# Kernel tuning notes

Measured on AMD Instinct MI355X. Metric: run time of the kernel, lower is better.

The kernel has to match this reference:

```python
import jax, jax.numpy as jnp
import numpy as np

VOCAB, HIDDEN, BATCH, EMB, SEQ = 512, 512, 64, 256, 1024


def _lstm_cell(x, h, c, Wih, Whh, bih, bhh):
    # PyTorch LSTMCell gate order: i, f, g, o
    gates = x @ Wih.T + bih + h @ Whh.T + bhh  # [B, 4H]
    i, f, g, o = jnp.split(gates, 4, axis=-1)
    i = jax.nn.sigmoid(i)
    f = jax.nn.sigmoid(f)
    g = jnp.tanh(g)
    o = jax.nn.sigmoid(o)
    c_new = f * c + i * g
    h_new = o * jnp.tanh(c_new)
    return h_new, c_new


def setup_inputs() -> dict:
    key = jax.random.key(0)
    ks = jax.random.split(key, 12)
    s_e = 1.0 / np.sqrt(HIDDEN)
    inp = {
        "x": jax.random.randint(ks[0], (SEQ, BATCH), 0, VOCAB, dtype=jnp.int64)
        if jax.config.jax_enable_x64 else jax.random.randint(ks[0], (SEQ, BATCH), 0, VOCAB, dtype=jnp.int32),
        "h0": jnp.zeros((BATCH, HIDDEN), jnp.float32),
        "c0": jnp.zeros((BATCH, HIDDEN), jnp.float32),
        "emb": jax.random.normal(ks[1], (VOCAB, EMB), jnp.float32),
        "Wih1": jax.random.uniform(ks[2], (4 * HIDDEN, EMB), jnp.float32, -s_e, s_e),
        "Whh1": jax.random.uniform(ks[3], (4 * HIDDEN, HIDDEN), jnp.float32, -s_e, s_e),
        "bih1": jax.random.uniform(ks[4], (4 * HIDDEN,), jnp.float32, -s_e, s_e),
        "bhh1": jax.random.uniform(ks[5], (4 * HIDDEN,), jnp.float32, -s_e, s_e),
        "Wih2": jax.random.uniform(ks[6], (4 * HIDDEN, HIDDEN), jnp.float32, -s_e, s_e),
        "Whh2": jax.random.uniform(ks[7], (4 * HIDDEN, HIDDEN), jnp.float32, -s_e, s_e),
        "bih2": jax.random.uniform(ks[8], (4 * HIDDEN,), jnp.float32, -s_e, s_e),
        "bhh2": jax.random.uniform(ks[9], (4 * HIDDEN,), jnp.float32, -s_e, s_e),
        "Wfc": jax.random.uniform(ks[10], (VOCAB, HIDDEN), jnp.float32, -s_e, s_e),
        "bfc": jax.random.uniform(ks[11], (VOCAB,), jnp.float32, -s_e, s_e),
    }
    return inp


def reference(x, h0, c0, emb, Wih1, Whh1, bih1, bhh1, Wih2, Whh2, bih2, bhh2, Wfc, bfc):
    # Embedding lookup for the whole sequence: [S, B, E]
    x_emb = emb[x]

    def step(carry, xt):
        h1, c1, h2, c2 = carry
        h1, c1 = _lstm_cell(xt, h1, c1, Wih1, Whh1, bih1, bhh1)
        h2, c2 = _lstm_cell(h1, h2, c2, Wih2, Whh2, bih2, bhh2)
        return (h1, c1, h2, c2), h2

    # Both layers start from the same (h0, c0), matching the original hc1, hc2 = (hc, hc)
    _, h2_seq = jax.lax.scan(step, (h0, c0, h0, c0), x_emb)  # [S, B, H]
    # Dropout is identity in eval mode; output projection over all timesteps at once.
    out = jnp.einsum('sbh,vh->sbv', h2_seq, Wfc) + bfc  # [S, B, V]
    return out
```

## Files before the change

### kernel.cpp

```cpp
#include <hip/hip_runtime.h>

#define SEQn   1024
#define BATCHn 64
#define EMBn   256
#define HIDn   512
#define VOCn   512

#define NGRP 4
#define NL1g 16
#define NL2g 16
#define NFCg 16
#define GBLK (NL1g + NL2g + NFCg)
#define NBLK (NGRP * GBLK)
#define NPHASE (SEQn + 2)
#define HS 8192
#define NSLOT 4
#define THR_IGN (-1)

using f16   = _Float16;
using half8 = __attribute__((ext_vector_type(8))) _Float16;
using f32x4 = __attribute__((ext_vector_type(4))) float;
using i32x4 = __attribute__((ext_vector_type(4))) int;

#define WS_FLG 0
#define WS_H1  4096
#define WS_H2  (WS_H1 + NGRP * NSLOT * 2 * HS * 2)
#define WS_P1  (WS_H2 + NGRP * NSLOT * 2 * HS * 2)


__device__ __forceinline__ float sigm_(float v) { return 1.0f / (1.0f + __expf(-v)); }
__device__ __forceinline__ float tanh_(float v) { return 1.0f - 2.0f / (__expf(2.0f * v) + 1.0f); }

__device__ __forceinline__ void st_b128_sc1(f16* p, f32x4 v) {
  asm volatile("global_store_dwordx4 %0, %1, off sc1" :: "v"(p), "v"(v) : "memory");
}

__device__ __forceinline__ void ld2_sc1(const f16* base, half8 (&a)[2]) {
  f32x4 t0, t1;
  asm volatile(
    "global_load_dwordx4 %0, %2, off sc1\n\t"
    "global_load_dwordx4 %1, %2, off offset:1024 sc1\n\t"
    "s_waitcnt vmcnt(0)"
    : "=&v"(t0), "=&v"(t1) : "v"(base) : "memory");
  a[0] = __builtin_bit_cast(half8, t0);
  a[1] = __builtin_bit_cast(half8, t1);
}
__device__ __forceinline__ void ld4_sc1(const f16* base, half8 (&a)[4]) {
  f32x4 t0, t1, t2, t3;
  asm volatile(
    "global_load_dwordx4 %0, %4, off sc1\n\t"
    "global_load_dwordx4 %1, %4, off offset:1024 sc1\n\t"
    "global_load_dwordx4 %2, %4, off offset:2048 sc1\n\t"
    "global_load_dwordx4 %3, %4, off offset:3072 sc1\n\t"
    "s_waitcnt vmcnt(0)"
    : "=&v"(t0), "=&v"(t1), "=&v"(t2), "=&v"(t3) : "v"(base) : "memory");
  a[0] = __builtin_bit_cast(half8, t0);
  a[1] = __builtin_bit_cast(half8, t1);
  a[2] = __builtin_bit_cast(half8, t2);
  a[3] = __builtin_bit_cast(half8, t3);
}

__global__ void k_init(const float* __restrict__ h0, char* __restrict__ ws) {
  int i = blockIdx.x * 256 + threadIdx.x;
  f16* h1b = (f16*)(ws + WS_H1);
  f16* h2b = (f16*)(ws + WS_H2);
  int g = i >> 13;
  int off = i & (HS - 1);
  int ks = off >> 9, rem = off & 511;
  int qq = rem >> 7, cc = (rem >> 3) & 15, e = rem & 7;
  int row = g * 16 + cc, col = ks * 32 + qq * 8 + e;
  f16 v = (f16)h0[row * HIDn + col];
  int base = g * (NSLOT * 2 * HS);
  h1b[base + off] = v;  h1b[base + HS + off] = v;
  h2b[base + off] = v;  h2b[base + HS + off] = v;
  if (i < 256) ((int*)ws)[i] = 0;
}

__global__ void k_p1(const float* __restrict__ emb, const float* __restrict__ Wih1,
                     const float* __restrict__ bih1, const float* __restrict__ bhh1,
                     char* __restrict__ ws) {
  __shared__ float elds[32 * 256];
  int tid = threadIdx.x;
  int vb = blockIdx.x >> 5, gb = blockIdx.x & 31;
  for (int i = tid; i < 32 * 256; i += 256) elds[i] = emb[vb * 32 * 256 + i];
  __syncthreads();
  int gl = tid & 63, vs = tid >> 6;
  int g = gb * 64 + gl;
  float bias = bih1[g] + bhh1[g];
  float acc[8];
#pragma unroll
  for (int r = 0; r < 8; ++r) acc[r] = bias;
  const float* wrow = Wih1 + g * EMBn;
#pragma unroll 4
  for (int e = 0; e < EMBn; ++e) {
    float w = wrow[e];
#pragma unroll
    for (int r = 0; r < 8; ++r) acc[r] += elds[(vs * 8 + r) * 256 + e] * w;
  }
  f16* P1 = (f16*)(ws + WS_P1);
#pragma unroll
  for (int r = 0; r < 8; ++r) P1[(vb * 32 + vs * 8 + r) * 2048 + g] = (f16)acc[r];
}

__global__ void __launch_bounds__(512, 2)
k_lstm(const int* __restrict__ x, const float* __restrict__ c0,
       const float* __restrict__ Whh1,
       const float* __restrict__ Wih2, const float* __restrict__ Whh2,
       const float* __restrict__ bih2, const float* __restrict__ bhh2,
       const float* __restrict__ Wfc, const float* __restrict__ bfc,
       float* __restrict__ out, char* __restrict__ ws)
{
  __shared__ float part[8][16][132];
  __shared__ alignas(16) f16 hstage[16][32];

  const int bid = blockIdx.x, tid = threadIdx.x;
  const int lane = tid & 63, wv = tid >> 6;
  const int cc = lane & 15, qq = lane >> 4;
  const int group = bid / GBLK, role = bid % GBLK;

  f16* h1g = (f16*)(ws + WS_H1) + group * (NSLOT * 2 * HS);
  f16* h2g = (f16*)(ws + WS_H2) + group * (NSLOT * 2 * HS);
  const f16* P1 = (const f16*)(ws + WS_P1);
  const int cls = (role < NL1g) ? 0 : (role < NL1g + NL2g) ? 1 : 2;
  int* flagp = (int*)ws + (group << 6) + (cls << 4) + (role & 15);

  half8 bfr[32];
  float cst = 0.f;
  float biasr[4] = {0.f, 0.f, 0.f, 0.f};
  float bfcr = 0.f;
  float pgf[4] = {0.f, 0.f, 0.f, 0.f};
  int j0 = 0;
  const int erow = tid >> 5, eu = tid & 31;

  if (cls == 0) {
    j0 = role * 32;
#pragma unroll
    for (int nt = 0; nt < 8; ++nt) {
      const float* wr = Whh1 + ((nt >> 1) * 512 + j0 + (nt & 1) * 16 + cc) * HIDn;
#pragma unroll
      for (int kk = 0; kk < 2; ++kk) {
        const float* s = wr + (wv * 2 + kk) * 32 + qq * 8;
        half8 hv;
#pragma unroll
        for (int j = 0; j < 8; ++j) hv[j] = (f16)s[j];
        bfr[nt * 2 + kk] = hv;
      }
    }
    cst = c0[(group * 16 + erow) * HIDn + j0 + eu];
    {
      const f16* pr = P1 + (size_t)x[group * 16 + erow] * 2048 + j0 + eu;
#pragma unroll
      for (int g = 0; g < 4; ++g) pgf[g] = (float)pr[g * 512];
    }
  } else if (cls == 1) {
    j0 = (role - NL1g) * 32;
    const int kh = wv >> 2, kq = wv & 3;
    const float* W = kh ? Whh2 : Wih2;
#pragma unroll
    for (int nt = 0; nt < 8; ++nt) {
      const float* wr = W + ((nt >> 1) * 512 + j0 + (nt & 1) * 16 + cc) * HIDn;
#pragma unroll
      for (int kk = 0; kk < 4; ++kk) {
        const float* s = wr + (kq * 4 + kk) * 32 + qq * 8;
        half8 hv;
#pragma unroll
        for (int j = 0; j < 8; ++j) hv[j] = (f16)s[j];
        bfr[nt * 4 + kk] = hv;
      }
    }
#pragma unroll
    for (int g = 0; g < 4; ++g)
      biasr[g] = bih2[g * 512 + j0 + eu] + bhh2[g * 512 + j0 + eu];
    cst = c0[(group * 16 + erow) * HIDn + j0 + eu];
  } else {
    j0 = (role - NL1g - NL2g) * 32;
#pragma unroll
    for (int nt = 0; nt < 2; ++nt) {
      const float* wr = Wfc + (j0 + nt * 16 + cc) * HIDn;
#pragma unroll
      for (int kk = 0; kk < 2; ++kk) {
        const float* s = wr + (wv * 2 + kk) * 32 + qq * 8;
        half8 hv;
#pragma unroll
        for (int j = 0; j < 8; ++j) hv[j] = (f16)s[j];
        bfr[nt * 2 + kk] = hv;
      }
    }
    bfcr = bfc[j0 + eu];
  }
  const int ks0 = j0 >> 5;
  __syncthreads();

  for (int p = 1; p <= NPHASE; ++p) {
    if (cls == 0) {
      if (p <= SEQn) {
        const f16* hp = h1g + ((p - 1) & 3) * (2 * HS);
        half8 a[2];
        ld2_sc1(hp + wv * 1024 + lane * 8, a);
        f32x4 acc[8];
#pragma unroll
        for (int nt = 0; nt < 8; ++nt)
#pragma unroll
          for (int r = 0; r < 4; ++r) acc[nt][r] = 0.f;
#pragma unroll
        for (int kk = 0; kk < 2; ++kk)
#pragma unroll
          for (int nt = 0; nt < 8; ++nt)
            acc[nt] = __builtin_amdgcn_mfma_f32_16x16x32_f16(a[kk], bfr[nt * 2 + kk], acc[nt], 0, 0, 0);
#pragma unroll
        for (int nt = 0; nt < 8; ++nt)
#pragma unroll
          for (int r = 0; r < 4; ++r)
            part[wv][qq * 4 + r][nt * 16 + cc] = acc[nt][r];
        __syncthreads();
        {
          float gs[4];
#pragma unroll
          for (int g = 0; g < 4; ++g) {
            float s = pgf[g];
#pragma unroll
            for (int kw = 0; kw < 8; ++kw) s += part[kw][erow][g * 32 + eu];
            gs[g] = s;
          }
          float cn = sigm_(gs[1]) * cst + sigm_(gs[0]) * tanh_(gs[2]);
          cst = cn;
          hstage[erow][eu] = (f16)(sigm_(gs[3]) * tanh_(cn));
        }
        __syncthreads();
        if (tid < 64) {
          f32x4 w = *(const f32x4*)&hstage[tid & 15][(tid >> 4) * 8];
          f16* ho = h1g + (p & 3) * (2 * HS) + ks0 * 512 + tid * 8;
          st_b128_sc1(ho, w);
          st_b128_sc1(ho + HS, w);
        }
      }
    } else if (cls == 1) {
      if (p >= 2 && p <= SEQn + 1) {
        const int kh = wv >> 2, kq = wv & 3;
        const f16* src = kh ? h2g + ((p - 2) & 3) * (2 * HS)
                            : h1g + ((p - 1) & 3) * (2 * HS) + HS;
        half8 a[4];
        ld4_sc1(src + kq * 2048 + lane * 8, a);
        f32x4 acc[8];
#pragma unroll
        for (int nt = 0; nt < 8; ++nt)
#pragma unroll
          for (int r = 0; r < 4; ++r) acc[nt][r] = 0.f;
#pragma unroll
        for (int kk = 0; kk < 4; ++kk)
#pragma unroll
          for (int nt = 0; nt < 8; ++nt)
            acc[nt] = __builtin_amdgcn_mfma_f32_16x16x32_f16(a[kk], bfr[nt * 4 + kk], acc[nt], 0, 0, 0);
#pragma unroll
        for (int nt = 0; nt < 8; ++nt)
#pragma unroll
          for (int r = 0; r < 4; ++r)
            part[wv][qq * 4 + r][nt * 16 + cc] = acc[nt][r];
        __syncthreads();
        {
          float gs[4];
#pragma unroll
          for (int g = 0; g < 4; ++g) {
            float s = biasr[g];
#pragma unroll
            for (int kw = 0; kw < 8; ++kw) s += part[kw][erow][g * 32 + eu];
            gs[g] = s;
          }
          float cn = sigm_(gs[1]) * cst + sigm_(gs[0]) * tanh_(gs[2]);
          cst = cn;
          hstage[erow][eu] = (f16)(sigm_(gs[3]) * tanh_(cn));
        }
        __syncthreads();
        if (tid < 64) {
          f32x4 w = *(const f32x4*)&hstage[tid & 15][(tid >> 4) * 8];
          f16* ho = h2g + ((p - 1) & 3) * (2 * HS) + ks0 * 512 + tid * 8;
          st_b128_sc1(ho, w);
          st_b128_sc1(ho + HS, w);
        }
      }
    } else {
      if (p >= 3) {
        const f16* hp = h2g + ((p - 2) & 3) * (2 * HS) + HS;
        half8 a[2];
        ld2_sc1(hp + wv * 1024 + lane * 8, a);
        f32x4 acc[2];
#pragma unroll
        for (int nt = 0; nt < 2; ++nt)
#pragma unroll
          for (int r = 0; r < 4; ++r) acc[nt][r] = 0.f;
#pragma unroll
        for (int kk = 0; kk < 2; ++kk)
#pragma unroll
          for (int nt = 0; nt < 2; ++nt)
            acc[nt] = __builtin_amdgcn_mfma_f32_16x16x32_f16(a[kk], bfr[nt * 2 + kk], acc[nt], 0, 0, 0);
#pragma unroll
        for (int nt = 0; nt < 2; ++nt)
#pragma unroll
          for (int r = 0; r < 4; ++r)
            part[wv][qq * 4 + r][nt * 16 + cc] = acc[nt][r];
        __syncthreads();
        {
          float s = bfcr;
#pragma unroll
          for (int kw = 0; kw < 8; ++kw) s += part[kw][erow][eu];
          float* op = out + (size_t)(p - 3) * (BATCHn * VOCn)
                    + (group * 16 + erow) * VOCn + j0 + eu;
          __builtin_nontemporal_store(s, op);
        }
      }
    }

    if (tid == 0) {
      if (cls != 2) asm volatile("s_waitcnt vmcnt(0)" ::: "memory");
      asm volatile("global_store_dword %0, %1, off sc1" :: "v"(flagp), "v"(p) : "memory");
    }
    if (cls == 0 && p < SEQn) {
      const f16* pr = P1 + (size_t)x[p * 64 + group * 16 + erow] * 2048 + j0 + eu;
#pragma unroll
      for (int g = 0; g < 4; ++g) pgf[g] = (float)pr[g * 512];
    }
    if (wv == 0) {
      int line = lane >> 2;
      int lc = (line < 3) ? line : 0;
      const int* fp = (const int*)ws + (group << 6) + (lc << 4) + ((lane & 3) << 2);
      int thr;
      if (cls == 0)      thr = (line == 0) ? p : (line == 1 ? p - 2 : THR_IGN);
      else if (cls == 1) thr = (line == 0) ? p : (line == 1 ? p : (line == 2 ? p - 2 : THR_IGN));
      else               thr = (line == 1) ? p : THR_IGN;
      if (line >= 3) thr = THR_IGN;
      for (;;) {
        i32x4 f;
        asm volatile("global_load_dwordx4 %0, %1, off sc1\n\ts_waitcnt vmcnt(0)"
                     : "=v"(f) : "v"(fp) : "memory");
        int ok = (f[0] >= thr) & (f[1] >= thr) & (f[2] >= thr) & (f[3] >= thr);
        if (__all(ok)) break;
        __builtin_amdgcn_s_sleep(1);
      }
    }
    __syncthreads();
  }
}

extern "C" void kernel_launch(void* const* d_in, const int* in_sizes, int n_in,
                              void* d_out, int out_size, void* d_ws, size_t ws_size,
                              hipStream_t stream) {
  (void)in_sizes; (void)n_in; (void)out_size; (void)ws_size;
  const int*   x    = (const int*)  d_in[0];
  const float* h0   = (const float*)d_in[1];
  const float* c0   = (const float*)d_in[2];
  const float* emb  = (const float*)d_in[3];
  const float* Wih1 = (const float*)d_in[4];
  const float* Whh1 = (const float*)d_in[5];
  const float* bih1 = (const float*)d_in[6];
  const float* bhh1 = (const float*)d_in[7];
  const float* Wih2 = (const float*)d_in[8];
  const float* Whh2 = (const float*)d_in[9];
  const float* bih2 = (const float*)d_in[10];
  const float* bhh2 = (const float*)d_in[11];
  const float* Wfc  = (const float*)d_in[12];
  const float* bfc  = (const float*)d_in[13];
  char* ws = (char*)d_ws;

  hipLaunchKernelGGL(k_init, dim3(128), dim3(256), 0, stream, h0, ws);
  hipLaunchKernelGGL(k_p1,   dim3(512), dim3(256), 0, stream, emb, Wih1, bih1, bhh1, ws);
  hipLaunchKernelGGL(k_lstm, dim3(NBLK), dim3(512), 0, stream,
                     x, c0, Whh1, Wih2, Whh2, bih2, bhh2, Wfc, bfc,
                     (float*)d_out, ws);
}
```

Measured before the change: 4.951 ms.

## Deepen hidden-state ring, drop duplicate stores, and make every wave poll flags independently

The hidden-state ring grows from 4 double-copied slots to 8 single-copy slots, and the anti-overwrite wait on consumers is relaxed from p-2 to p-6. Each block now reuses its own freshly computed slice from shared memory instead of waiting on its own flag. All waves poll the flags themselves instead of wave 0 followed by a block barrier. The flag store and h store rotate across waves, and the flag store no longer waits on vmcnt. The goal is to cut per-step barrier and handshake latency on the recurrent critical path. The risk is memory-ordering problems, since the flag may become visible before the h data from other lanes or waves.

After: 6.525 ms. +31.8%, slower.

```diff
diff --git a/kernel.cpp b/kernel.cpp
--- a/kernel.cpp
+++ b/kernel.cpp
@@ -14,7 +14,7 @@
 #define NBLK (NGRP * GBLK)
 #define NPHASE (SEQn + 2)
 #define HS 8192
-#define NSLOT 4
+#define NSLOT 8
 #define THR_IGN (-1)
 
 using f16   = _Float16;
@@ -24,8 +24,8 @@
 
 #define WS_FLG 0
 #define WS_H1  4096
-#define WS_H2  (WS_H1 + NGRP * NSLOT * 2 * HS * 2)
-#define WS_P1  (WS_H2 + NGRP * NSLOT * 2 * HS * 2)
+#define WS_H2  (WS_H1 + NGRP * NSLOT * HS * 2)
+#define WS_P1  (WS_H2 + NGRP * NSLOT * HS * 2)
 
 
 __device__ __forceinline__ float sigm_(float v) { return 1.0f / (1.0f + __expf(-v)); }
@@ -70,9 +70,9 @@
   int qq = rem >> 7, cc = (rem >> 3) & 15, e = rem & 7;
   int row = g * 16 + cc, col = ks * 32 + qq * 8 + e;
   f16 v = (f16)h0[row * HIDn + col];
-  int base = g * (NSLOT * 2 * HS);
-  h1b[base + off] = v;  h1b[base + HS + off] = v;
-  h2b[base + off] = v;  h2b[base + HS + off] = v;
+  int base = g * (NSLOT * HS);
+  h1b[base + off] = v;
+  h2b[base + off] = v;
   if (i < 256) ((int*)ws)[i] = 0;
 }
 
@@ -118,11 +118,12 @@
   const int cc = lane & 15, qq = lane >> 4;
   const int group = bid / GBLK, role = bid % GBLK;
 
-  f16* h1g = (f16*)(ws + WS_H1) + group * (NSLOT * 2 * HS);
-  f16* h2g = (f16*)(ws + WS_H2) + group * (NSLOT * 2 * HS);
+  f16* h1g = (f16*)(ws + WS_H1) + group * (NSLOT * HS);
+  f16* h2g = (f16*)(ws + WS_H2) + group * (NSLOT * HS);
   const f16* P1 = (const f16*)(ws + WS_P1);
   const int cls = (role < NL1g) ? 0 : (role < NL1g + NL2g) ? 1 : 2;
-  int* flagp = (int*)ws + (group << 6) + (cls << 4) + (role & 15);
+  const int owni = role & 15;
+  int* flagp = (int*)ws + (group << 6) + (cls << 4) + owni;
 
   half8 bfr[32];
   float cst = 0.f;
@@ -192,11 +193,18 @@
   __syncthreads();
 
   for (int p = 1; p <= NPHASE; ++p) {
-    if (cls == 0) {
-      if (p <= SEQn) {
-        const f16* hp = h1g + ((p - 1) & 3) * (2 * HS);
+    const int act = (cls == 0) ? (p <= SEQn)
+                  : (cls == 1) ? (p >= 2 && p <= SEQn + 1)
+                               : (p >= 3);
+    if (act) {
+      if (cls == 0) {
+        const f16* hp = h1g + ((p - 1) & 7) * HS;
         half8 a[2];
         ld2_sc1(hp + wv * 1024 + lane * 8, a);
+        if (p >= 2 && wv == (ks0 >> 1)) {
+          half8 sub = *(const half8*)&hstage[cc][qq * 8];
+          if ((ks0 & 1) == 0) a[0] = sub; else a[1] = sub;
+        }
         f32x4 acc[8];
 #pragma unroll
         for (int nt = 0; nt < 8; ++nt)
@@ -212,35 +220,20 @@
 #pragma unroll
           for (int r = 0; r < 4; ++r)
             part[wv][qq * 4 + r][nt * 16 + cc] = acc[nt][r];
-        __syncthreads();
-        {
-          float gs[4];
-#pragma unroll
-          for (int g = 0; g < 4; ++g) {
-            float s = pgf[g];
-#pragma unroll
-            for (int kw = 0; kw < 8; ++kw) s += part[kw][erow][g * 32 + eu];
-            gs[g] = s;
-          }
-          float cn = sigm_(gs[1]) * cst + sigm_(gs[0]) * tanh_(gs[2]);
-          cst = cn;
-          hstage[erow][eu] = (f16)(sigm_(gs[3]) * tanh_(cn));
-        }
-        __syncthreads();
-        if (tid < 64) {
-          f32x4 w = *(const f32x4*)&hstage[tid & 15][(tid >> 4) * 8];
-          f16* ho = h1g + (p & 3) * (2 * HS) + ks0 * 512 + tid * 8;
-          st_b128_sc1(ho, w);
-          st_b128_sc1(ho + HS, w);
-        }
-      }
-    } else if (cls == 1) {
-      if (p >= 2 && p <= SEQn + 1) {
+      } else if (cls == 1) {
         const int kh = wv >> 2, kq = wv & 3;
-        const f16* src = kh ? h2g + ((p - 2) & 3) * (2 * HS)
-                            : h1g + ((p - 1) & 3) * (2 * HS) + HS;
+        const f16* src = kh ? h2g + ((p - 2) & 7) * HS
+                            : h1g + ((p - 1) & 7) * HS;
         half8 a[4];
         ld4_sc1(src + kq * 2048 + lane * 8, a);
+        if (p >= 3 && kh == 1 && kq == (ks0 >> 2)) {
+          half8 sub = *(const half8*)&hstage[cc][qq * 8];
+          int k3 = ks0 & 3;
+          if (k3 == 0) a[0] = sub;
+          else if (k3 == 1) a[1] = sub;
+          else if (k3 == 2) a[2] = sub;
+          else a[3] = sub;
+        }
         f32x4 acc[8];
 #pragma unroll
         for (int nt = 0; nt < 8; ++nt)
@@ -256,31 +249,8 @@
 #pragma unroll
           for (int r = 0; r < 4; ++r)
             part[wv][qq * 4 + r][nt * 16 + cc] = acc[nt][r];
-        __syncthreads();
-        {
-          float gs[4];
-#pragma unroll
-          for (int g = 0; g < 4; ++g) {
-            float s = biasr[g];
-#pragma unroll
-            for (int kw = 0; kw < 8; ++kw) s += part[kw][erow][g * 32 + eu];
-            gs[g] = s;
-          }
-          float cn = sigm_(gs[1]) * cst + sigm_(gs[0]) * tanh_(gs[2]);
-          cst = cn;
-          hstage[erow][eu] = (f16)(sigm_(gs[3]) * tanh_(cn));
-        }
-        __syncthreads();
-        if (tid < 64) {
-          f32x4 w = *(const f32x4*)&hstage[tid & 15][(tid >> 4) * 8];
-          f16* ho = h2g + ((p - 1) & 3) * (2 * HS) + ks0 * 512 + tid * 8;
-          st_b128_sc1(ho, w);
-          st_b128_sc1(ho + HS, w);
-        }
-      }
-    } else {
-      if (p >= 3) {
-        const f16* hp = h2g + ((p - 2) & 3) * (2 * HS) + HS;
+      } else {
+        const f16* hp = h2g + ((p - 2) & 7) * HS;
         half8 a[2];
         ld2_sc1(hp + wv * 1024 + lane * 8, a);
         f32x4 acc[2];
@@ -298,46 +268,73 @@
 #pragma unroll
           for (int r = 0; r < 4; ++r)
             part[wv][qq * 4 + r][nt * 16 + cc] = acc[nt][r];
-        __syncthreads();
-        {
-          float s = bfcr;
-#pragma unroll
-          for (int kw = 0; kw < 8; ++kw) s += part[kw][erow][eu];
-          float* op = out + (size_t)(p - 3) * (BATCHn * VOCn)
-                    + (group * 16 + erow) * VOCn + j0 + eu;
-          __builtin_nontemporal_store(s, op);
+      }
+    }
+    __syncthreads();
+    if (act) {
+      if (cls != 2) {
+        float gs[4];
+#pragma unroll
+        for (int g = 0; g < 4; ++g) {
+          float s = (cls == 0) ? pgf[g] : biasr[g];
+#pragma unroll
+          for (int kw = 0; kw < 8; ++kw) s += part[kw][erow][g * 32 + eu];
+          gs[g] = s;
         }
-      }
-    }
-
-    if (tid == 0) {
-      if (cls != 2) asm volatile("s_waitcnt vmcnt(0)" ::: "memory");
-      asm volatile("global_store_dword %0, %1, off sc1" :: "v"(flagp), "v"(p) : "memory");
-    }
-    if (cls == 0 && p < SEQn) {
-      const f16* pr = P1 + (size_t)x[p * 64 + group * 16 + erow] * 2048 + j0 + eu;
-#pragma unroll
-      for (int g = 0; g < 4; ++g) pgf[g] = (float)pr[g * 512];
-    }
-    if (wv == 0) {
+        float cn = sigm_(gs[1]) * cst + sigm_(gs[0]) * tanh_(gs[2]);
+        cst = cn;
+        hstage[erow][eu] = (f16)(sigm_(gs[3]) * tanh_(cn));
+      } else {
+        float s = bfcr;
+#pragma unroll
+        for (int kw = 0; kw < 8; ++kw) s += part[kw][erow][eu];
+        float* op = out + (size_t)(p - 3) * (BATCHn * VOCn)
+                  + (group * 16 + erow) * VOCn + j0 + eu;
+        __builtin_nontemporal_store(s, op);
+      }
+    }
+    __syncthreads();
+
+    const int duty = p & 7;
+    if (act && cls != 2 && wv == duty) {
+      f32x4 w = *(const f32x4*)&hstage[lane & 15][(lane >> 4) * 8];
+      f16* ho = ((cls == 0) ? h1g + (p & 7) * HS : h2g + ((p - 1) & 7) * HS)
+              + ks0 * 512 + lane * 8;
+      st_b128_sc1(ho, w);
+    }
+    {
       int line = lane >> 2;
       int lc = (line < 3) ? line : 0;
       const int* fp = (const int*)ws + (group << 6) + (lc << 4) + ((lane & 3) << 2);
       int thr;
-      if (cls == 0)      thr = (line == 0) ? p : (line == 1 ? p - 2 : THR_IGN);
-      else if (cls == 1) thr = (line == 0) ? p : (line == 1 ? p : (line == 2 ? p - 2 : THR_IGN));
+      if (cls == 0)      thr = (line == 0) ? p : (line == 1 ? p - 6 : THR_IGN);
+      else if (cls == 1) thr = (line == 0) ? p : (line == 1 ? p : (line == 2 ? p - 6 : THR_IGN));
       else               thr = (line == 1) ? p : THR_IGN;
       if (line >= 3) thr = THR_IGN;
-      for (;;) {
-        i32x4 f;
-        asm volatile("global_load_dwordx4 %0, %1, off sc1\n\ts_waitcnt vmcnt(0)"
-                     : "=v"(f) : "v"(fp) : "memory");
-        int ok = (f[0] >= thr) & (f[1] >= thr) & (f[2] >= thr) & (f[3] >= thr);
-        if (__all(ok)) break;
-        __builtin_amdgcn_s_sleep(1);
-      }
-    }
-    __syncthreads();
+      const int exj = (line == cls && (lane & 3) == (owni >> 2)) ? (owni & 3) : -1;
+      i32x4 f;
+      asm volatile("global_load_dwordx4 %0, %1, off sc1\n\ts_waitcnt vmcnt(0)"
+                   : "=&v"(f) : "v"(fp) : "memory");
+      if (wv == duty && lane == 0)
+        asm volatile("global_store_dword %0, %1, off sc1"
+                     :: "v"(flagp), "v"(p) : "memory");
+      if (cls == 0 && p < SEQn) {
+        const f16* pr = P1 + (size_t)x[p * 64 + group * 16 + erow] * 2048 + j0 + eu;
+#pragma unroll
+        for (int g = 0; g < 4; ++g) pgf[g] = (float)pr[g * 512];
+      }
+      if (p < NPHASE) {
+        int ok = ((f[0] >= thr) | (exj == 0)) & ((f[1] >= thr) | (exj == 1))
+               & ((f[2] >= thr) | (exj == 2)) & ((f[3] >= thr) | (exj == 3));
+        while (!__all(ok)) {
+          __builtin_amdgcn_s_sleep(1);
+          asm volatile("global_load_dwordx4 %0, %1, off sc1\n\ts_waitcnt vmcnt(0)"
+                       : "=&v"(f) : "v"(fp) : "memory");
+          ok = ((f[0] >= thr) | (exj == 0)) & ((f[1] >= thr) | (exj == 1))
+             & ((f[2] >= thr) | (exj == 2)) & ((f[3] >= thr) | (exj == 3));
+        }
+      }
+    }
   }
 }
 
```
